# Optimization experiments

Measured on AMD Instinct MI355X. Metric: run time of the kernel, lower is better.

The kernel has to match this reference:

```python
import jax, jax.numpy as jnp
import numpy as np

CHANNELS = 512
NUM_HEADS = 8
GROUPS = 32
EPS = 1e-5


def setup_inputs() -> dict:
    key = jax.random.key(0)
    ks = jax.random.split(key, 7)
    C = CHANNELS
    x = jax.random.normal(ks[0], (8, C, 32, 32), dtype=jnp.float32)
    gn_weight = jnp.ones((C,), dtype=jnp.float32)
    gn_bias = jnp.zeros((C,), dtype=jnp.float32)
    # Conv1d(C, 3C, k=1) weights ~ N(0, 0.02) per init_weights
    qkv_w = 0.02 * jax.random.normal(ks[1], (3 * C, C), dtype=jnp.float32)
    qkv_b = 0.01 * jax.random.normal(ks[2], (3 * C,), dtype=jnp.float32)
    out_w = 0.02 * jax.random.normal(ks[3], (C, C), dtype=jnp.float32)
    out_b = 0.01 * jax.random.normal(ks[4], (C,), dtype=jnp.float32)
    return {"x": x, "gn_weight": gn_weight, "gn_bias": gn_bias,
            "qkv_w": qkv_w, "qkv_b": qkv_b, "out_w": out_w, "out_b": out_b}


def _forward(x, gn_weight, gn_bias, qkv_w, qkv_b, out_w, out_b):
    n, c, h, w = x.shape
    hw = h * w
    heads = NUM_HEADS
    cph = c // heads
    xs = x.reshape(n, c, hw)  # [N, C, HW]
    # GroupNorm over (channels-in-group, spatial)
    xg = xs.reshape(n, GROUPS, c // GROUPS, hw)
    mean = jnp.mean(xg, axis=(2, 3), keepdims=True)
    var = jnp.var(xg, axis=(2, 3), keepdims=True)
    xn = ((xg - mean) * jax.lax.rsqrt(var + EPS)).reshape(n, c, hw)
    xn = xn * gn_weight[None, :, None] + gn_bias[None, :, None]
    # 1x1 Conv1d QKV projection
    qkv = jnp.einsum('oc,ncl->nol', qkv_w, xn) + qkv_b[None, :, None]  # [N, 3C, HW]
    q, k, v = jnp.split(qkv, 3, axis=1)  # each [N, C, HW]
    q = q.reshape(n * heads, cph, hw)
    k = k.reshape(n * heads, cph, hw)
    v = v.reshape(n * heads, cph, hw)
    scale = 1.0 / np.sqrt(cph).astype(np.float32)
    scores = jnp.einsum('bci,bcj->bij', q, k) * scale  # [NH, HW, HW]
    attn = jax.nn.softmax(scores, axis=-1)
    weighted = jnp.einsum('bij,bcj->bic', attn, v)  # [NH, HW, cph]
    # Faithful to torch: reshape(n, -1, h, w) on [n*heads, hw, cph] layout
    weighted = weighted.reshape(n, c, h, w)
    out = jnp.einsum('oc,nchw->nohw', out_w, weighted) + out_b[None, :, None, None]
    return out


def reference(x, gn_weight, gn_bias, qkv_w, qkv_b, out_w, out_b):
    return _forward(x, gn_weight, gn_bias, qkv_w, qkv_b, out_w, out_b)
```

## Files before the change

### kernel.cpp

```cpp
#include <hip/hip_runtime.h>
#include <math.h>

#define N_    8
#define C_    512
#define HW_   1024
#define G_    32
#define CPG_  16
#define OC3_  1536
#define LOG2E 1.44269504f

typedef _Float16 f16;
typedef f16 f16x8 __attribute__((ext_vector_type(8)));
typedef f16 f16x4 __attribute__((ext_vector_type(4)));
typedef f16 f16x2 __attribute__((ext_vector_type(2)));
typedef float f32x4 __attribute__((ext_vector_type(4)));
typedef float f32x16 __attribute__((ext_vector_type(16)));

#if __has_builtin(__builtin_amdgcn_exp2f)
#define EXP2F(x) __builtin_amdgcn_exp2f(x)
#else
#define EXP2F(x) exp2f(x)
#endif

#define GLOAD_LDS16(g, l)                                                          \
    __builtin_amdgcn_global_load_lds(                                              \
        (const __attribute__((address_space(1))) unsigned int*)(const void*)(g),   \
        (__attribute__((address_space(3))) unsigned int*)(void*)(l), 16, 0, 0)

#define WAIT_VM0() __builtin_amdgcn_s_waitcnt(0x0F70)

__global__ __launch_bounds__(256) void prep(const float* __restrict__ x,
                                            const float* __restrict__ gw,
                                            const float* __restrict__ gb,
                                            f16* __restrict__ XT,
                                            const float* __restrict__ qkv_w,
                                            const float* __restrict__ out_w,
                                            const float* __restrict__ qkv_b,
                                            f16* __restrict__ Wq,
                                            f16* __restrict__ Wo,
                                            float* __restrict__ qkv_bs) {
    __shared__ float red1[4], red2[4];
    __shared__ float sm, srstd;
    if (blockIdx.x >= 256) {
        const float QS = 0.125f * LOG2E;
        int idx = (blockIdx.x - 256) * 256 + threadIdx.x;
        if (idx < 786432) {
            float v = qkv_w[idx];
            if (idx < 262144) v *= QS;
            Wq[idx] = (f16)v;
        } else if (idx < 786432 + 262144) {
            Wo[idx - 786432] = (f16)out_w[idx - 786432];
        } else if (idx < 786432 + 262144 + 1536) {
            int i = idx - 786432 - 262144;
            float v = qkv_b[i];
            if (i < 512) v *= QS;
            qkv_bs[i] = v;
        }
        return;
    }
    int blk = blockIdx.x;
    int n = blk >> 5, g = blk & 31;
    size_t base = ((size_t)n * C_ + (size_t)g * CPG_) * HW_;
    const float4* xp4 = (const float4*)(x + base);
    float4 vals[16];
    float s1 = 0.f, s2 = 0.f;
#pragma unroll
    for (int r = 0; r < 16; r++) {
        float4 v = xp4[r * 256 + threadIdx.x];
        vals[r] = v;
        s1 += v.x + v.y + v.z + v.w;
        s2 += v.x * v.x + v.y * v.y + v.z * v.z + v.w * v.w;
    }
#pragma unroll
    for (int off = 32; off > 0; off >>= 1) {
        s1 += __shfl_down(s1, off, 64);
        s2 += __shfl_down(s2, off, 64);
    }
    int wave = threadIdx.x >> 6, lane = threadIdx.x & 63;
    if (lane == 0) { red1[wave] = s1; red2[wave] = s2; }
    __syncthreads();
    if (threadIdx.x == 0) {
        float t1 = red1[0] + red1[1] + red1[2] + red1[3];
        float t2 = red2[0] + red2[1] + red2[2] + red2[3];
        float mean = t1 * (1.f / 16384.f);
        float var  = t2 * (1.f / 16384.f) - mean * mean;
        sm = mean;
        srstd = rsqrtf(var + 1e-5f);
    }
    __syncthreads();
    float mean = sm, rstd = srstd;
    float av[16], bbv[16];
#pragma unroll
    for (int r = 0; r < 16; r++) {
        int c = g * CPG_ + r;
        av[r] = gw[c] * rstd;
        bbv[r] = gb[c] - mean * av[r];
    }
    f16x8 lo[4], hi[4];
#pragma unroll
    for (int r = 0; r < 16; r++) {
        float4 v = vals[r];
        float a = av[r], bb = bbv[r];
        f16 e0 = (f16)(v.x * a + bb), e1 = (f16)(v.y * a + bb);
        f16 e2 = (f16)(v.z * a + bb), e3 = (f16)(v.w * a + bb);
        if (r < 8) { lo[0][r] = e0; lo[1][r] = e1; lo[2][r] = e2; lo[3][r] = e3; }
        else { hi[0][r - 8] = e0; hi[1][r - 8] = e1; hi[2][r - 8] = e2; hi[3][r - 8] = e3; }
    }
    f16* xt = XT + (size_t)n * C_ * HW_ + ((size_t)g * HW_ + threadIdx.x * 4) * 16;
#pragma unroll
    for (int comp = 0; comp < 4; comp++) {
        *(f16x8*)&xt[comp * 16]     = lo[comp];
        *(f16x8*)&xt[comp * 16 + 8] = hi[comp];
    }
}

template <bool FINAL>
__global__ __launch_bounds__(256, 4) void gemm_f16(const f16* __restrict__ A,
                                                   const f16* __restrict__ B,
                                                   const float* __restrict__ bias,
                                                   void* __restrict__ Yq,
                                                   f16* __restrict__ Yv) {
    constexpr int BM = FINAL ? 64 : 128;
    constexpr int MI = BM / 32;
    constexpr int ABUF = BM * 32 * 2;
    constexpr int BBUF = 128 * 32 * 2;
    constexpr int G = (BM / 64) + 2;
    __shared__ __align__(16) unsigned char smem[3 * ABUF + 3 * BBUF];
    int tid = threadIdx.x, lane = tid & 63, w = tid >> 6;
    int m = lane & 15, quad = lane >> 4;
    int ow0 = (w & 1) * (BM / 2), lw0 = (w >> 1) * 64;
    int flat = blockIdx.x;
    int n = flat & 7, rest = flat >> 3;
    int l0 = (rest & 7) * 128, o0 = (rest >> 3) * BM;
    const f16* Bn = B + (size_t)n * C_ * HW_;

    f32x4 acc[MI][4];
#pragma unroll
    for (int i = 0; i < MI; i++)
#pragma unroll
        for (int j = 0; j < 4; j++)
#pragma unroll
            for (int r = 0; r < 4; r++) acc[i][j][r] = 0.f;

#define STAGE_STEP(c0_, pb_)                                                       \
    do {                                                                           \
        _Pragma("unroll")                                                          \
        for (int it = 0; it < BM / 64; it++) {                                     \
            int q = it * 256 + tid;                                                \
            int row = q >> 2, sg = (q & 3) ^ ((row >> 1) & 3);                     \
            GLOAD_LDS16(A + (size_t)(o0 + row) * 512 + (c0_) + sg * 8,             \
                        (f16*)(smem + (pb_) * ABUF) + (size_t)(it * 256 + w * 64) * 8); \
        }                                                                          \
        _Pragma("unroll")                                                          \
        for (int it = 0; it < 2; it++) {                                           \
            int q = it * 256 + tid;                                                \
            int row = q >> 2, sg = (q & 3) ^ ((row >> 1) & 3);                     \
            size_t baddr;                                                          \
            if (FINAL) {                                                           \
                baddr = (size_t)(l0 + row) * 512 + (c0_) + sg * 8;                 \
            } else {                                                               \
                int c = (c0_) + sg * 8;                                            \
                baddr = ((size_t)(c >> 4) * HW_ + (l0 + row)) * 16 + (c & 15);     \
            }                                                                      \
            GLOAD_LDS16(Bn + baddr,                                                \
                        (f16*)(smem + 3 * ABUF + (pb_) * BBUF) +                   \
                            (size_t)(it * 256 + w * 64) * 8);                      \
        }                                                                          \
    } while (0)

    STAGE_STEP(0, 0);
    STAGE_STEP(32, 1);

    for (int cs = 0; cs < 16; cs++) {
        int p = cs % 3;
        if (cs < 15) __builtin_amdgcn_s_waitcnt(0x0F70 | G);
        else         WAIT_VM0();
        __builtin_amdgcn_s_barrier();
        if (cs + 2 < 16) STAGE_STEP((cs + 2) * 32, (cs + 2) % 3);
        const f16* Asp = (const f16*)(smem + p * ABUF);
        const f16* Bsp = (const f16*)(smem + 3 * ABUF + p * BBUF);
        f16x8 af[MI], bf[4];
#pragma unroll
        for (int ib = 0; ib < MI; ib++) {
            int row = ow0 + ib * 16 + m;
            int sg = quad ^ ((row >> 1) & 3);
            af[ib] = *(const f16x8*)&Asp[row * 32 + sg * 8];
        }
#pragma unroll
        for (int jb = 0; jb < 4; jb++) {
            int row = lw0 + jb * 16 + m;
            int sg = quad ^ ((row >> 1) & 3);
            bf[jb] = *(const f16x8*)&Bsp[row * 32 + sg * 8];
        }
        __builtin_amdgcn_s_setprio(1);
#pragma unroll
        for (int ib = 0; ib < MI; ib++)
#pragma unroll
            for (int jb = 0; jb < 4; jb++)
                acc[ib][jb] = __builtin_amdgcn_mfma_f32_16x16x32_f16(
                    af[ib], bf[jb], acc[ib][jb], 0, 0, 0);
        __builtin_amdgcn_s_setprio(0);
    }
#undef STAGE_STEP

    float bv[MI][4];
#pragma unroll
    for (int ib = 0; ib < MI; ib++)
#pragma unroll
        for (int r = 0; r < 4; r++)
            bv[ib][r] = bias[o0 + ow0 + ib * 16 + quad * 4 + r];

    if (FINAL) {
        float* on = (float*)Yq + (size_t)n * C_ * HW_;
#pragma unroll
        for (int ib = 0; ib < MI; ib++)
#pragma unroll
            for (int jb = 0; jb < 4; jb++)
#pragma unroll
                for (int r = 0; r < 4; r++)
                    on[(size_t)(o0 + ow0 + ib * 16 + quad * 4 + r) * HW_ +
                       l0 + lw0 + jb * 16 + m] = acc[ib][jb][r] + bv[ib][r];
    } else if (o0 >= 1024) {
        int mp = (m & 3) | ((m & 4) << 1) | ((m & 8) >> 1);
        f16* vn = Yv + (size_t)n * C_ * HW_;
#pragma unroll
        for (int ib = 0; ib < MI; ib++)
#pragma unroll
            for (int jb = 0; jb < 4; jb++)
#pragma unroll
                for (int r = 0; r < 4; r++)
                    vn[(size_t)(o0 - 1024 + ow0 + ib * 16 + quad * 4 + r) * HW_ +
                       l0 + lw0 + jb * 16 + mp] = (f16)(acc[ib][jb][r] + bv[ib][r]);
    } else {
        __syncthreads();
        f16* T = (f16*)smem;
#pragma unroll
        for (int ib = 0; ib < MI; ib++)
#pragma unroll
            for (int jb = 0; jb < 4; jb++) {
                f16x4 h;
#pragma unroll
                for (int r = 0; r < 4; r++) h[r] = (f16)(acc[ib][jb][r] + bv[ib][r]);
                int l = lw0 + jb * 16 + m;
                int oo = ow0 + ib * 16 + quad * 4;
                *(f16x4*)&T[l * 136 + oo] = h;
            }
        __syncthreads();
        f16* qn = (f16*)Yq + (size_t)n * HW_ * 1024;
#pragma unroll
        for (int rep = 0; rep < 8; rep++) {
            int idx = rep * 256 + tid;
            int l = idx >> 4, seg = idx & 15;
            f16x8 v = *(const f16x8*)&T[l * 136 + seg * 8];
            *(f16x8*)&qn[(size_t)(l0 + l) * 1024 + o0 + seg * 8] = v;
        }
    }
}

__global__ __launch_bounds__(256, 2) void attn_f16(const f16* __restrict__ qkvT,
                                                   const f16* __restrict__ vbuf,
                                                   f16* __restrict__ w2T) {
    __shared__ __align__(16) unsigned char smem[49152];
    f16* LDSo = (f16*)smem;

    int tid = threadIdx.x;
    int lane = tid & 63, wave = tid >> 6;
    int l31 = lane & 31, hi = lane >> 5;
    int flat = blockIdx.x;
    int xcd = flat & 7, slot = flat >> 3;
    int itile = slot >> 3, bh = (slot & 7) * 8 + xcd;
    int n = bh >> 3, head = bh & 7;
    int i0 = itile * 128;
    const f16* qb = qkvT + (size_t)n * HW_ * 1024 + head * 64;
    const f16* kb = qb + 512;
    const f16* vb = vbuf + (size_t)n * C_ * HW_ + (size_t)head * 64 * HW_;

    f16x8 aq[4];
    {
        const f16* qr = qb + (size_t)(i0 + wave * 32 + l31) * 1024;
#pragma unroll
        for (int dc = 0; dc < 4; dc++)
            aq[dc] = *(const f16x8*)&qr[dc * 16 + hi * 8];
    }

#define STAGE_KV(j0_, pb_)                                                         \
    do {                                                                           \
        _Pragma("unroll")                                                          \
        for (int it = 0; it < 2; it++) {                                           \
            int chunk = it * 256 + tid;                                            \
            int row = chunk >> 3, seg = chunk & 7;                                 \
            int segg = seg ^ (row & 7);                                            \
            GLOAD_LDS16(kb + (size_t)((j0_) + row) * 1024 + segg * 8,              \
                        (f16*)(smem + (pb_) * 8192) +                              \
                            ((size_t)it * 256 + wave * 64) * 8);                   \
            GLOAD_LDS16(vb + (size_t)row * HW_ + (j0_) + segg * 8,                 \
                        (f16*)(smem + 24576 + (pb_) * 8192) +                      \
                            ((size_t)it * 256 + wave * 64) * 8);                   \
        }                                                                          \
    } while (0)

    STAGE_KV(0, 0);
    STAGE_KV(64, 1);

    f32x16 oaccD[2], oaccL;
#pragma unroll
    for (int r = 0; r < 16; r++) { oaccD[0][r] = 0.f; oaccD[1][r] = 0.f; oaccL[r] = 0.f; }
    const f16x8 vones = {(f16)1.f, (f16)1.f, (f16)1.f, (f16)1.f,
                         (f16)1.f, (f16)1.f, (f16)1.f, (f16)1.f};

    for (int jt = 0; jt < 16; jt++) {
        int p = jt % 3;
        if (jt < 15) __builtin_amdgcn_s_waitcnt(0x0F74);
        else         WAIT_VM0();
        __builtin_amdgcn_s_barrier();
        if (jt + 2 < 16) STAGE_KV((jt + 2) * 64, (jt + 2) % 3);
        const f16* Kp = (const f16*)(smem + p * 8192);
        const f16* Vp = (const f16*)(smem + 24576 + p * 8192);

        f32x16 s0, s1;
#pragma unroll
        for (int r = 0; r < 16; r++) { s0[r] = 0.f; s1[r] = 0.f; }
        __builtin_amdgcn_s_setprio(1);
#pragma unroll
        for (int dc = 0; dc < 4; dc++) {
            int row0 = l31, row1 = 32 + l31;
            int seg = dc * 2 + hi;
            f16x8 kf0 = *(const f16x8*)&Kp[row0 * 64 + ((seg ^ (row0 & 7)) * 8)];
            f16x8 kf1 = *(const f16x8*)&Kp[row1 * 64 + ((seg ^ (row1 & 7)) * 8)];
            s0 = __builtin_amdgcn_mfma_f32_32x32x16_f16(kf0, aq[dc], s0, 0, 0, 0);
            s1 = __builtin_amdgcn_mfma_f32_32x32x16_f16(kf1, aq[dc], s1, 0, 0, 0);
        }
        __builtin_amdgcn_s_setprio(0);

        f16x8 pfc[4];
#pragma unroll
        for (int q = 0; q < 4; q++) {
            f32x16 sv = (q < 2) ? s0 : s1;
            int bs = (q & 1) * 8;
#pragma unroll
            for (int t = 0; t < 4; t++) {
                float a = EXP2F(sv[bs + 2 * t]);
                float b = EXP2F(sv[bs + 2 * t + 1]);
                f16x2 pk = __builtin_bit_cast(f16x2, __builtin_amdgcn_cvt_pkrtz(a, b));
                pfc[q][2 * t]     = pk[0];
                pfc[q][2 * t + 1] = pk[1];
            }
        }

        __builtin_amdgcn_s_setprio(1);
#pragma unroll
        for (int q = 0; q < 4; q++) {
            oaccL = __builtin_amdgcn_mfma_f32_32x32x16_f16(vones, pfc[q],
                                                           oaccL, 0, 0, 0);
#pragma unroll
            for (int t = 0; t < 2; t++) {
                int c = t * 32 + l31;
                int seg = q * 2 + hi;
                f16x8 vf = *(const f16x8*)&Vp[c * 64 + ((seg ^ (c & 7)) * 8)];
                oaccD[t] = __builtin_amdgcn_mfma_f32_32x32x16_f16(vf, pfc[q],
                                                                  oaccD[t], 0, 0, 0);
            }
        }
        __builtin_amdgcn_s_setprio(0);
    }
#undef STAGE_KV

    float linv = 1.f / oaccL[0];

    WAIT_VM0();
    __syncthreads();
#pragma unroll
    for (int t = 0; t < 2; t++)
#pragma unroll
        for (int r = 0; r < 16; r++) {
            int cc = t * 32 + (r & 3) + 8 * (r >> 2) + 4 * hi;
            int il = wave * 32 + l31;
            int sc = (il & 15) * 64 + cc;
            LDSo[sc * 8 + (il >> 4)] = (f16)(oaccD[t][r] * linv);
        }
    __syncthreads();
    f16* w2n = w2T + (size_t)n * HW_ * 512;
    int chbase = head * 64 + itile * 8;
#pragma unroll
    for (int it = 0; it < 4; it++) {
        int sc = it * 256 + tid;
        *(f16x8*)&w2n[(size_t)sc * 512 + chbase] = *(const f16x8*)&LDSo[sc * 8];
    }
}

extern "C" void kernel_launch(void* const* d_in, const int* in_sizes, int n_in,
                              void* d_out, int out_size, void* d_ws, size_t ws_size,
                              hipStream_t stream) {
    (void)in_sizes; (void)n_in; (void)out_size; (void)ws_size;
    const float* x     = (const float*)d_in[0];
    const float* gw    = (const float*)d_in[1];
    const float* gb    = (const float*)d_in[2];
    const float* qkv_w = (const float*)d_in[3];
    const float* qkv_b = (const float*)d_in[4];
    const float* out_w = (const float*)d_in[5];
    const float* out_b = (const float*)d_in[6];
    float* out = (float*)d_out;
    char* ws = (char*)d_ws;

    const size_t MB = 1024 * 1024;
    f16*   qkvT   = (f16*)ws;
    f16*   XT     = (f16*)(ws + 16 * MB);
    f16*   vbuf   = (f16*)(ws + 24 * MB);
    f16*   w2T    = (f16*)(ws + 32 * MB);
    f16*   Wq     = (f16*)(ws + 40 * MB);
    f16*   Wo     = (f16*)(ws + 42 * MB);
    float* qkv_bs = (float*)(ws + 43 * MB);

    prep<<<dim3(256 + 4103), 256, 0, stream>>>(x, gw, gb, XT,
                                               qkv_w, out_w, qkv_b, Wq, Wo, qkv_bs);
    gemm_f16<false><<<dim3(768), 256, 0, stream>>>(Wq, XT, qkv_bs, (void*)qkvT, vbuf);
    attn_f16<<<dim3(512), 256, 0, stream>>>(qkvT, vbuf, w2T);
    gemm_f16<true><<<dim3(512), 256, 0, stream>>>(Wo, w2T, out_b, (void*)out, nullptr);
}
```

Measured before the change: 138.4 us.

## Double query rows per attention block to reuse K/V fragments across two Q tiles

Each attention wave now processes 64 query rows as two 32-row groups that share the same K and V fragments read from LDS. Each block therefore covers 256 rows and the grid is halved. This cuts LDS fragment reads and K/V staging per query row. The K/V pipeline drops from three LDS stages to two, with a full vmcnt wait before every barrier, and launch bounds allow only one block per CU. That means fewer resident waves and more registers per thread, which risks weaker latency hiding and less overlap between loads and compute.

```diff
diff --git a/kernel.cpp b/kernel.cpp
--- a/kernel.cpp
+++ b/kernel.cpp
@@ -257,10 +257,10 @@
     }
 }
 
-__global__ __launch_bounds__(256, 2) void attn_f16(const f16* __restrict__ qkvT,
+__global__ __launch_bounds__(256, 1) void attn_f16(const f16* __restrict__ qkvT,
                                                    const f16* __restrict__ vbuf,
                                                    f16* __restrict__ w2T) {
-    __shared__ __align__(16) unsigned char smem[49152];
+    __shared__ __align__(16) unsigned char smem[32768];
     f16* LDSo = (f16*)smem;
 
     int tid = threadIdx.x;
@@ -270,17 +270,20 @@
     int xcd = flat & 7, slot = flat >> 3;
     int itile = slot >> 3, bh = (slot & 7) * 8 + xcd;
     int n = bh >> 3, head = bh & 7;
-    int i0 = itile * 128;
+    int i0 = itile * 256;
     const f16* qb = qkvT + (size_t)n * HW_ * 1024 + head * 64;
     const f16* kb = qb + 512;
     const f16* vb = vbuf + (size_t)n * C_ * HW_ + (size_t)head * 64 * HW_;
 
-    f16x8 aq[4];
+    f16x8 aqA[4], aqB[4];
     {
-        const f16* qr = qb + (size_t)(i0 + wave * 32 + l31) * 1024;
-#pragma unroll
-        for (int dc = 0; dc < 4; dc++)
-            aq[dc] = *(const f16x8*)&qr[dc * 16 + hi * 8];
+        const f16* qrA = qb + (size_t)(i0 + wave * 64 + l31) * 1024;
+        const f16* qrB = qrA + 32 * 1024;
+#pragma unroll
+        for (int dc = 0; dc < 4; dc++) {
+            aqA[dc] = *(const f16x8*)&qrA[dc * 16 + hi * 8];
+            aqB[dc] = *(const f16x8*)&qrB[dc * 16 + hi * 8];
+        }
     }
 
 #define STAGE_KV(j0_, pb_)                                                         \
@@ -294,32 +297,34 @@
                         (f16*)(smem + (pb_) * 8192) +                              \
                             ((size_t)it * 256 + wave * 64) * 8);                   \
             GLOAD_LDS16(vb + (size_t)row * HW_ + (j0_) + segg * 8,                 \
-                        (f16*)(smem + 24576 + (pb_) * 8192) +                      \
+                        (f16*)(smem + 16384 + (pb_) * 8192) +                      \
                             ((size_t)it * 256 + wave * 64) * 8);                   \
         }                                                                          \
     } while (0)
 
     STAGE_KV(0, 0);
-    STAGE_KV(64, 1);
-
-    f32x16 oaccD[2], oaccL;
-#pragma unroll
-    for (int r = 0; r < 16; r++) { oaccD[0][r] = 0.f; oaccD[1][r] = 0.f; oaccL[r] = 0.f; }
+
+    f32x16 dA0, dA1, dB0, dB1, lA, lB;
+#pragma unroll
+    for (int r = 0; r < 16; r++) {
+        dA0[r] = 0.f; dA1[r] = 0.f; dB0[r] = 0.f; dB1[r] = 0.f;
+        lA[r] = 0.f;  lB[r] = 0.f;
+    }
     const f16x8 vones = {(f16)1.f, (f16)1.f, (f16)1.f, (f16)1.f,
                          (f16)1.f, (f16)1.f, (f16)1.f, (f16)1.f};
 
     for (int jt = 0; jt < 16; jt++) {
-        int p = jt % 3;
-        if (jt < 15) __builtin_amdgcn_s_waitcnt(0x0F74);
-        else         WAIT_VM0();
-        __builtin_amdgcn_s_barrier();
-        if (jt + 2 < 16) STAGE_KV((jt + 2) * 64, (jt + 2) % 3);
+        int p = jt & 1;
         const f16* Kp = (const f16*)(smem + p * 8192);
-        const f16* Vp = (const f16*)(smem + 24576 + p * 8192);
-
-        f32x16 s0, s1;
-#pragma unroll
-        for (int r = 0; r < 16; r++) { s0[r] = 0.f; s1[r] = 0.f; }
+        const f16* Vp = (const f16*)(smem + 16384 + p * 8192);
+        WAIT_VM0();
+        __syncthreads();
+        if (jt < 15) STAGE_KV((jt + 1) * 64, 1 - p);
+
+        f32x16 sA0, sA1, sB0, sB1;
+#pragma unroll
+        for (int r = 0; r < 16; r++) { sA0[r] = 0.f; sA1[r] = 0.f;
+                                       sB0[r] = 0.f; sB1[r] = 0.f; }
         __builtin_amdgcn_s_setprio(1);
 #pragma unroll
         for (int dc = 0; dc < 4; dc++) {
@@ -327,64 +332,85 @@
             int seg = dc * 2 + hi;
             f16x8 kf0 = *(const f16x8*)&Kp[row0 * 64 + ((seg ^ (row0 & 7)) * 8)];
             f16x8 kf1 = *(const f16x8*)&Kp[row1 * 64 + ((seg ^ (row1 & 7)) * 8)];
-            s0 = __builtin_amdgcn_mfma_f32_32x32x16_f16(kf0, aq[dc], s0, 0, 0, 0);
-            s1 = __builtin_amdgcn_mfma_f32_32x32x16_f16(kf1, aq[dc], s1, 0, 0, 0);
+            sA0 = __builtin_amdgcn_mfma_f32_32x32x16_f16(kf0, aqA[dc], sA0, 0, 0, 0);
+            sB0 = __builtin_amdgcn_mfma_f32_32x32x16_f16(kf0, aqB[dc], sB0, 0, 0, 0);
+            sA1 = __builtin_amdgcn_mfma_f32_32x32x16_f16(kf1, aqA[dc], sA1, 0, 0, 0);
+            sB1 = __builtin_amdgcn_mfma_f32_32x32x16_f16(kf1, aqB[dc], sB1, 0, 0, 0);
         }
         __builtin_amdgcn_s_setprio(0);
 
-        f16x8 pfc[4];
+        f16x8 pfA[4], pfB[4];
 #pragma unroll
         for (int q = 0; q < 4; q++) {
-            f32x16 sv = (q < 2) ? s0 : s1;
+            f32x16 svA = (q < 2) ? sA0 : sA1;
+            f32x16 svB = (q < 2) ? sB0 : sB1;
             int bs = (q & 1) * 8;
 #pragma unroll
             for (int t = 0; t < 4; t++) {
-                float a = EXP2F(sv[bs + 2 * t]);
-                float b = EXP2F(sv[bs + 2 * t + 1]);
-                f16x2 pk = __builtin_bit_cast(f16x2, __builtin_amdgcn_cvt_pkrtz(a, b));
-                pfc[q][2 * t]     = pk[0];
-                pfc[q][2 * t + 1] = pk[1];
+                float a0 = EXP2F(svA[bs + 2 * t]);
+                float a1 = EXP2F(svA[bs + 2 * t + 1]);
+                f16x2 pkA = __builtin_bit_cast(f16x2, __builtin_amdgcn_cvt_pkrtz(a0, a1));
+                pfA[q][2 * t]     = pkA[0];
+                pfA[q][2 * t + 1] = pkA[1];
+                float b0 = EXP2F(svB[bs + 2 * t]);
+                float b1 = EXP2F(svB[bs + 2 * t + 1]);
+                f16x2 pkB = __builtin_bit_cast(f16x2, __builtin_amdgcn_cvt_pkrtz(b0, b1));
+                pfB[q][2 * t]     = pkB[0];
+                pfB[q][2 * t + 1] = pkB[1];
             }
         }
 
         __builtin_amdgcn_s_setprio(1);
 #pragma unroll
         for (int q = 0; q < 4; q++) {
-            oaccL = __builtin_amdgcn_mfma_f32_32x32x16_f16(vones, pfc[q],
-                                                           oaccL, 0, 0, 0);
+            lA = __builtin_amdgcn_mfma_f32_32x32x16_f16(vones, pfA[q], lA, 0, 0, 0);
+            lB = __builtin_amdgcn_mfma_f32_32x32x16_f16(vones, pfB[q], lB, 0, 0, 0);
 #pragma unroll
             for (int t = 0; t < 2; t++) {
                 int c = t * 32 + l31;
                 int seg = q * 2 + hi;
                 f16x8 vf = *(const f16x8*)&Vp[c * 64 + ((seg ^ (c & 7)) * 8)];
-                oaccD[t] = __builtin_amdgcn_mfma_f32_32x32x16_f16(vf, pfc[q],
-                                                                  oaccD[t], 0, 0, 0);
+                if (t == 0) {
+                    dA0 = __builtin_amdgcn_mfma_f32_32x32x16_f16(vf, pfA[q], dA0, 0, 0, 0);
+                    dB0 = __builtin_amdgcn_mfma_f32_32x32x16_f16(vf, pfB[q], dB0, 0, 0, 0);
+                } else {
+                    dA1 = __builtin_amdgcn_mfma_f32_32x32x16_f16(vf, pfA[q], dA1, 0, 0, 0);
+                    dB1 = __builtin_amdgcn_mfma_f32_32x32x16_f16(vf, pfB[q], dB1, 0, 0, 0);
+                }
             }
         }
         __builtin_amdgcn_s_setprio(0);
     }
 #undef STAGE_KV
 
-    float linv = 1.f / oaccL[0];
+    float linvA = 1.f / lA[0];
+    float linvB = 1.f / lB[0];
 
     WAIT_VM0();
     __syncthreads();
 #pragma unroll
-    for (int t = 0; t < 2; t++)
-#pragma unroll
-        for (int r = 0; r < 16; r++) {
-            int cc = t * 32 + (r & 3) + 8 * (r >> 2) + 4 * hi;
-            int il = wave * 32 + l31;
-            int sc = (il & 15) * 64 + cc;
-            LDSo[sc * 8 + (il >> 4)] = (f16)(oaccD[t][r] * linv);
-        }
+    for (int grp = 0; grp < 2; grp++)
+#pragma unroll
+        for (int t = 0; t < 2; t++)
+#pragma unroll
+            for (int r = 0; r < 16; r++) {
+                int cc = t * 32 + (r & 3) + 8 * (r >> 2) + 4 * hi;
+                int il = wave * 64 + grp * 32 + l31;
+                int sc = (il & 15) * 64 + cc;
+                float val;
+                if (grp == 0) val = (t == 0 ? dA0[r] : dA1[r]) * linvA;
+                else          val = (t == 0 ? dB0[r] : dB1[r]) * linvB;
+                LDSo[sc * 16 + (il >> 4)] = (f16)val;
+            }
     __syncthreads();
     f16* w2n = w2T + (size_t)n * HW_ * 512;
-    int chbase = head * 64 + itile * 8;
-#pragma unroll
-    for (int it = 0; it < 4; it++) {
-        int sc = it * 256 + tid;
-        *(f16x8*)&w2n[(size_t)sc * 512 + chbase] = *(const f16x8*)&LDSo[sc * 8];
+    int chbase = head * 64 + itile * 16;
+#pragma unroll
+    for (int it = 0; it < 8; it++) {
+        int idx = it * 256 + tid;
+        int sc = idx >> 1, half = idx & 1;
+        *(f16x8*)&w2n[(size_t)sc * 512 + chbase + half * 8] =
+            *(const f16x8*)&LDSo[sc * 16 + half * 8];
     }
 }
 
@@ -414,6 +440,6 @@
     prep<<<dim3(256 + 4103), 256, 0, stream>>>(x, gw, gb, XT,
                                                qkv_w, out_w, qkv_b, Wq, Wo, qkv_bs);
     gemm_f16<false><<<dim3(768), 256, 0, stream>>>(Wq, XT, qkv_bs, (void*)qkvT, vbuf);
-    attn_f16<<<dim3(512), 256, 0, stream>>>(qkvT, vbuf, w2T);
+    attn_f16<<<dim3(256), 256, 0, stream>>>(qkvT, vbuf, w2T);
     gemm_f16<true><<<dim3(512), 256, 0, stream>>>(Wo, w2T, out_b, (void*)out, nullptr);
 }
```

Measured after the change: 142.7 us. 1.03x slower.
